# Optimization experiments

Measured on AMD Instinct MI355X. Metric: run time of the kernel, lower is better.

The kernel has to match this reference:

```python
import jax, jax.numpy as jnp
import numpy as np

NUM_HEADS = 16


def setup_inputs() -> dict:
    key = jax.random.key(0)
    k1, k2, k3 = jax.random.split(key, 3)
    B, N, C = 4, 2048, 1024
    x = jax.random.normal(k1, (B, N, C), dtype=jnp.float32)
    w_qkv = jax.random.normal(k2, (C, 3 * C), dtype=jnp.float32) * (C ** -0.5)
    w_proj = jax.random.normal(k3, (C, C), dtype=jnp.float32) * (C ** -0.5)
    b_proj = jnp.zeros((C,), dtype=jnp.float32)
    return {"x": x, "w_qkv": w_qkv, "w_proj": w_proj, "b_proj": b_proj}


def reference(x, w_qkv, w_proj, b_proj):
    B, N, C = x.shape
    H = NUM_HEADS
    hd = C // H
    scale = hd ** -0.5
    # qkv projection (no bias), split into q, k, v per head
    qkv = jnp.einsum('bnc,cd->bnd', x, w_qkv)            # [B, N, 3C]
    qkv = qkv.reshape(B, N, 3, H, hd).transpose(0, 3, 2, 1, 4)  # [B, H, 3, N, hd]
    q, k, v = qkv[:, :, 0], qkv[:, :, 1], qkv[:, :, 2]   # each [B, H, N, hd]
    q = q * scale
    attn = jax.nn.softmax(jnp.einsum('bhnd,bhmd->bhnm', q, k), axis=-1)  # [B, H, N, N]
    out = jnp.einsum('bhnm,bhmd->bhnd', attn, v)         # [B, H, N, hd]
    out = out.transpose(0, 2, 1, 3).reshape(B, N, C)
    return jnp.einsum('bnc,cd->bnd', out, w_proj) + b_proj
```

## Files before the change

### kernel.cpp

```cpp
#include <hip/hip_runtime.h>

typedef short s16x8 __attribute__((ext_vector_type(8)));
typedef float f32x4 __attribute__((ext_vector_type(4)));
typedef float f32x16 __attribute__((ext_vector_type(16)));
typedef unsigned u32x4 __attribute__((ext_vector_type(4)));


__device__ __forceinline__ unsigned short bf16bits(float f) {
  unsigned u = __builtin_bit_cast(unsigned, f);
  unsigned rnd = 0x7FFFu + ((u >> 16) & 1u);
  return (unsigned short)((u + rnd) >> 16);
}

__device__ __forceinline__ unsigned pk_bf16(float lo, float hi) {
  unsigned r;
  asm("v_cvt_pk_bf16_f32 %0, %1, %2" : "=v"(r) : "v"(lo), "v"(hi));
  return r;
}

__device__ __forceinline__ void async16(const void* g, void* l) {
  __builtin_amdgcn_global_load_lds((const __attribute__((address_space(1))) void*)g,
                                   (__attribute__((address_space(3))) void*)l, 16, 0, 0);
}

__device__ __forceinline__ f32x4 mfma16(s16x8 a, s16x8 b, f32x4 c) {
  return __builtin_amdgcn_mfma_f32_16x16x32_bf16(a, b, c, 0, 0, 0);
}

__device__ __forceinline__ f32x16 mfma32(s16x8 a, s16x8 b, f32x16 c) {
  return __builtin_amdgcn_mfma_f32_32x32x16_bf16(a, b, c, 0, 0, 0);
}

__device__ __forceinline__ s16x8 lds_frag(const unsigned short* S, int row, int c8, int U) {
  int unit = row * U + (c8 ^ (row & (U - 1)));
  return *(const s16x8*)(S + unit * 8);
}

__global__ __launch_bounds__(256) void prep(const float4* __restrict__ x4,
                                            unsigned short* __restrict__ Xb,
                                            const float* __restrict__ w_qkv,
                                            unsigned short* __restrict__ Wqt,
                                            const float* __restrict__ w_proj,
                                            unsigned short* __restrict__ Wpt) {
  __shared__ float tile[32][33];
  const int blk = blockIdx.x, t = threadIdx.x;
  if (blk < 2048) {
    const int n4 = 8388608 / 4, stride = 2048 * 256;
    for (int i = blk * 256 + t; i < n4; i += stride) {
      float4 v = x4[i];
      uint2 o;
      o.x = pk_bf16(v.x, v.y);
      o.y = pk_bf16(v.z, v.w);
      *(uint2*)(Xb + (size_t)i * 4) = o;
    }
    return;
  }
  const float* in;
  unsigned short* out;
  int R, C, c0, r0;
  if (blk < 2048 + 3072) {
    int idx = blk - 2048;
    in = w_qkv; out = Wqt; R = 1024; C = 3072;
    c0 = (idx % 96) * 32; r0 = (idx / 96) * 32;
  } else {
    int idx = blk - (2048 + 3072);
    in = w_proj; out = Wpt; R = 1024; C = 1024;
    c0 = (idx & 31) * 32; r0 = (idx >> 5) * 32;
  }
  const int tx = t & 31, ty = t >> 5;
  #pragma unroll
  for (int i = 0; i < 32; i += 8)
    tile[ty + i][tx] = in[(size_t)(r0 + ty + i) * C + c0 + tx];
  __syncthreads();
  #pragma unroll
  for (int i = 0; i < 32; i += 8)
    out[(size_t)(c0 + ty + i) * R + r0 + tx] = bf16bits(tile[tx][ty + i]);
}

__global__ __launch_bounds__(256) void transpose_v(const unsigned short* __restrict__ V,
                                                   unsigned short* __restrict__ Vt) {
  __shared__ unsigned short sm[64 * 68];
  int bh = blockIdx.y, kt0 = blockIdx.x * 64;
  const unsigned short* v = V + (size_t)bh * 2048 * 64 + (size_t)kt0 * 64;
  unsigned short* vt = Vt + (size_t)bh * 64 * 2048;
  int t = threadIdx.x;
  #pragma unroll
  for (int i = 0; i < 4; ++i) {
    int u = i * 256 + t;
    int f = u * 4;
    int k = f >> 6, d0 = f & 63;
    *(uint2*)&sm[k * 68 + d0] = *(const uint2*)&v[f];
  }
  __syncthreads();
  #pragma unroll
  for (int j = 0; j < 16; ++j) {
    int o = j * 256 + t;
    int d = o >> 6, k = o & 63;
    vt[(size_t)d * 2048 + kt0 + k] = sm[k * 68 + d];
  }
}


template <typename EPI>
__global__ __launch_bounds__(512, 2) void gemm8(const unsigned short* __restrict__ A,
                                                const unsigned short* __restrict__ Bt,
                                                int K, EPI epi) {
  __shared__ __align__(16) unsigned short As[3 * 128 * 64];
  __shared__ __align__(16) unsigned short Bs[3 * 256 * 64];
  const int tid = threadIdx.x, wid = tid >> 6, lane = tid & 63;
  const int quad = lane >> 4, l16 = lane & 15;
  const int bm0 = blockIdx.y * 128, bn0 = blockIdx.x * 256;
  const int wm = (wid & 1) * 64, wn = (wid >> 1) * 64;
  const int NT = K >> 6;
  f32x4 acc[4][4] = {};

  const int srow = tid >> 3;
  const int sc8 = (tid & 7) ^ (srow & 7);
  auto stage = [&](int s, int tk, int k) {
    int col = tk * 64 + sc8 * 8;
    if (k < 2)
      async16(A + (size_t)(bm0 + k * 64 + srow) * K + col,
              (char*)As + s * 16384 + k * 8192 + wid * 1024);
    else
      async16(Bt + (size_t)(bn0 + (k - 2) * 64 + srow) * K + col,
              (char*)Bs + s * 32768 + (k - 2) * 8192 + wid * 1024);
  };

  #pragma unroll
  for (int k = 0; k < 6; ++k) stage(0, 0, k);
  #pragma unroll
  for (int k = 0; k < 6; ++k) stage(1, 1, k);
  asm volatile("s_waitcnt vmcnt(6)" ::: "memory");
  __builtin_amdgcn_s_barrier();
  __builtin_amdgcn_sched_barrier(0);

  int sc = 0;
  for (int t = 0; t < NT; ++t) {
    const unsigned short* as = As + sc * 8192;
    const unsigned short* bs = Bs + sc * 16384;
    const int sp = (sc == 0) ? 2 : sc - 1;
    const bool pf = (t + 2 < NT);

    #pragma unroll
    for (int kk = 0; kk < 2; ++kk) {
      s16x8 a[4], b[4];
      #pragma unroll
      for (int i = 0; i < 4; ++i) a[i] = lds_frag(as, wm + i * 16 + l16, kk * 4 + quad, 8);
      #pragma unroll
      for (int j = 0; j < 4; ++j) b[j] = lds_frag(bs, wn + j * 16 + l16, kk * 4 + quad, 8);
      if (pf) { stage(sp, t + 2, kk * 3 + 0); stage(sp, t + 2, kk * 3 + 1); stage(sp, t + 2, kk * 3 + 2); }
      __builtin_amdgcn_sched_barrier(0);
      __builtin_amdgcn_s_barrier();
      __builtin_amdgcn_s_setprio(1);
      #pragma unroll
      for (int i = 0; i < 4; ++i)
        #pragma unroll
        for (int j = 0; j < 4; ++j)
          acc[i][j] = mfma16(a[i], b[j], acc[i][j]);
      __builtin_amdgcn_s_setprio(0);
      __builtin_amdgcn_sched_barrier(0);
      if (kk == 1) {
        if (pf) asm volatile("s_waitcnt vmcnt(6)" ::: "memory");
        else    asm volatile("s_waitcnt vmcnt(0)" ::: "memory");
      }
      __builtin_amdgcn_s_barrier();
    }
    sc = (sc == 2) ? 0 : sc + 1;
  }

  #pragma unroll
  for (int i = 0; i < 4; ++i)
    #pragma unroll
    for (int j = 0; j < 4; ++j)
      epi.store4(bm0 + wm + i * 16 + quad * 4, bn0 + wn + j * 16 + l16, acc[i][j]);
}

struct QKVEpi {
  unsigned short *Q, *K, *V;
  float qscale;
  __device__ __forceinline__ void store4(int m0, int n, f32x4 v) const {
    int s = m0 >> 10, h = (m0 >> 6) & 15, d = m0 & 63;
    int b = n >> 11, ns = n & 2047;
    unsigned short* dst = (s == 0) ? Q : ((s == 1) ? K : V);
    float sc = (s == 0) ? qscale : 1.f;
    uint2 o;
    o.x = pk_bf16(v[0] * sc, v[1] * sc);
    o.y = pk_bf16(v[2] * sc, v[3] * sc);
    *(uint2*)&dst[(((size_t)b * 16 + h) * 2048 + ns) * 64 + d] = o;
  }
};

struct ProjEpi {
  const float* bias;
  float* out;
  __device__ __forceinline__ void store4(int m0, int n, f32x4 v) const {
    float4 b4 = *(const float4*)&bias[m0];
    float4 o = {v[0] + b4.x, v[1] + b4.y, v[2] + b4.z, v[3] + b4.w};
    *(float4*)&out[(size_t)n * 1024 + m0] = o;
  }
};

__global__ __launch_bounds__(256, 4) void flash_attn(const unsigned short* __restrict__ Q,
                                                     const unsigned short* __restrict__ K,
                                                     const unsigned short* __restrict__ Vt,
                                                     unsigned short* __restrict__ O) {
  __shared__ __align__(16) unsigned short Ks[2][8 * 512];
  __shared__ __align__(16) unsigned short Vs[2][8 * 512];
  const int tid = threadIdx.x, wid = tid >> 6, lane = tid & 63;
  const int l31 = lane & 31, half = lane >> 5;
  const int bid = blockIdx.y * gridDim.x + blockIdx.x;
  const int xcd = bid & 7, idx = bid >> 3;
  const int bh = xcd * 8 + (idx & 7);
  const int qt = idx >> 3;
  const unsigned short* Qg = Q + (size_t)bh * 2048 * 64;
  const unsigned short* Kg = K + (size_t)bh * 2048 * 64;
  const unsigned short* Vg = Vt + (size_t)bh * 64 * 2048;
  const int qrow = qt * 128 + wid * 32 + l31;

  s16x8 qB[4];
  #pragma unroll
  for (int s = 0; s < 4; ++s)
    qB[s] = *(const s16x8*)&Qg[(size_t)qrow * 64 + s * 16 + half * 8];

  const bool isK = wid < 2;
  int sA[4];
  #pragma unroll
  for (int t = 0; t < 4; ++t) {
    int c = (wid & 1) * 4 + t;
    if (isK) sA[t] = ((c >> 2) * 32 + l31) * 64 + ((c & 3) * 2 + half) * 8;
    else     sA[t] = ((c & 1) * 32 + l31) * 2048 + (c >> 1) * 16 + half * 8;
  }

  auto stage = [&](int kt, int buf) {
    const int kb = kt * 64;
    #pragma unroll
    for (int t = 0; t < 4; ++t) {
      int c = (wid & 1) * 4 + t;
      if (isK) async16(Kg + (size_t)kb * 64 + sA[t], (char*)&Ks[buf][0] + c * 1024);
      else     async16(Vg + kb + sA[t],              (char*)&Vs[buf][0] + c * 1024);
    }
  };

  f32x16 oacc[2] = {};
  float l_i = 0.f;
  const f32x16 fz = {};

  stage(0, 0);
  for (int kt = 0; kt < 32; ++kt) {
    const int cur = kt & 1;
    __syncthreads();
    if (kt + 1 < 32) stage(kt + 1, cur ^ 1);
    const unsigned short* ks = &Ks[cur][0];
    const unsigned short* vs = &Vs[cur][0];

    f32x16 st[2];
    __builtin_amdgcn_s_setprio(1);
    #pragma unroll
    for (int kf = 0; kf < 2; ++kf) {
      {
        s16x8 a = *(const s16x8*)&ks[((kf * 4 + 0) * 64 + lane) * 8];
        st[kf] = mfma32(a, qB[0], fz);
      }
      #pragma unroll
      for (int s = 1; s < 4; ++s) {
        s16x8 a = *(const s16x8*)&ks[((kf * 4 + s) * 64 + lane) * 8];
        st[kf] = mfma32(a, qB[s], st[kf]);
      }
    }
    __builtin_amdgcn_s_setprio(0);

    #pragma unroll
    for (int kf = 0; kf < 2; ++kf) {
      float a0 = 0.f, a1 = 0.f, a2 = 0.f, a3 = 0.f;
      #pragma unroll
      for (int r = 0; r < 16; r += 4) {
        float p0 = __builtin_amdgcn_exp2f(st[kf][r + 0]);
        float p1 = __builtin_amdgcn_exp2f(st[kf][r + 1]);
        float p2 = __builtin_amdgcn_exp2f(st[kf][r + 2]);
        float p3 = __builtin_amdgcn_exp2f(st[kf][r + 3]);
        st[kf][r + 0] = p0; st[kf][r + 1] = p1; st[kf][r + 2] = p2; st[kf][r + 3] = p3;
        a0 += p0; a1 += p1; a2 += p2; a3 += p3;
      }
      float rs = (a0 + a1) + (a2 + a3);
      rs += __shfl_xor(rs, 32);
      l_i += rs;
      #pragma unroll
      for (int t = 0; t < 2; ++t) {
        int rb = t * 8;
        unsigned pa0 = pk_bf16(st[kf][rb + 0], st[kf][rb + 1]);
        unsigned pa1 = pk_bf16(st[kf][rb + 2], st[kf][rb + 3]);
        unsigned pb0 = pk_bf16(st[kf][rb + 4], st[kf][rb + 5]);
        unsigned pb1 = pk_bf16(st[kf][rb + 6], st[kf][rb + 7]);
        unsigned s0 = half ? pa0 : pb0;
        unsigned s1 = half ? pa1 : pb1;
        unsigned r0 = (unsigned)__shfl_xor((int)s0, 32);
        unsigned r1 = (unsigned)__shfl_xor((int)s1, 32);
        u32x4 bP;
        bP[0] = half ? r0 : pa0;
        bP[1] = half ? r1 : pa1;
        bP[2] = half ? pb0 : r0;
        bP[3] = half ? pb1 : r1;
        __builtin_amdgcn_s_setprio(1);
        #pragma unroll
        for (int f = 0; f < 2; ++f) {
          s16x8 aV = *(const s16x8*)&vs[(((kf * 2 + t) * 2 + f) * 64 + lane) * 8];
          oacc[f] = mfma32(aV, __builtin_bit_cast(s16x8, bP), oacc[f]);
        }
        __builtin_amdgcn_s_setprio(0);
      }
    }
  }

  const int b = bh >> 4, h = bh & 15;
  float inv = 1.f / l_i;
  size_t base = (((size_t)b * 2048 + qrow) * 16 + h) * 64;
  #pragma unroll
  for (int f = 0; f < 2; ++f)
    #pragma unroll
    for (int q = 0; q < 4; ++q) {
      int d0 = f * 32 + q * 8 + half * 4;
      uint2 o;
      o.x = pk_bf16(oacc[f][q * 4 + 0] * inv, oacc[f][q * 4 + 1] * inv);
      o.y = pk_bf16(oacc[f][q * 4 + 2] * inv, oacc[f][q * 4 + 3] * inv);
      *(uint2*)&O[base + d0] = o;
    }
}


extern "C" void kernel_launch(void* const* d_in, const int* in_sizes, int n_in,
                              void* d_out, int out_size, void* d_ws, size_t ws_size,
                              hipStream_t stream) {
  (void)in_sizes; (void)n_in; (void)out_size; (void)ws_size;
  const float* x = (const float*)d_in[0];
  const float* w_qkv = (const float*)d_in[1];
  const float* w_proj = (const float*)d_in[2];
  const float* b_proj = (const float*)d_in[3];
  float* out = (float*)d_out;
  char* ws = (char*)d_ws;
  const size_t MB = 1ull << 20;
  unsigned short* Xb  = (unsigned short*)(ws);
  unsigned short* Wqt = (unsigned short*)(ws + 16 * MB);
  unsigned short* Wpt = (unsigned short*)(ws + 22 * MB);
  unsigned short* Qb  = (unsigned short*)(ws + 24 * MB);
  unsigned short* Kb  = (unsigned short*)(ws + 40 * MB);
  unsigned short* Vb  = (unsigned short*)(ws + 56 * MB);
  unsigned short* Vt  = Xb;
  unsigned short* Ob  = Vb;

  prep<<<2048 + 3072 + 1024, 256, 0, stream>>>((const float4*)x, Xb, w_qkv, Wqt, w_proj, Wpt);

  QKVEpi e1{Qb, Kb, Vb, 0.125f * 1.44269504088896340736f};
  gemm8<QKVEpi><<<dim3(32, 24), 512, 0, stream>>>(Wqt, Xb, 1024, e1);

  transpose_v<<<dim3(32, 64), 256, 0, stream>>>(Vb, Vt);
  flash_attn<<<dim3(16, 64), 256, 0, stream>>>(Qb, Kb, Vt, Ob);

  ProjEpi e2{b_proj, out};
  gemm8<ProjEpi><<<dim3(32, 8), 512, 0, stream>>>(Wpt, Ob, 1024, e2);
}
```

Baseline: 278.7 us.

## Process two 32-row query groups per wave in flash attention to reuse K/V fragments

Each wave now handles 64 query rows (two 32-row groups) instead of 32, so every K and V fragment read from LDS feeds two MFMAs. The query tile per block doubles to 256, the grid halves, and launch bounds drop to 2 blocks per CU to allow the extra registers. This cuts LDS traffic and K/V staging per query row, at the cost of higher register pressure, lower occupancy, and fewer blocks to fill the GPU.

```diff
diff --git a/kernel.cpp b/kernel.cpp
--- a/kernel.cpp
+++ b/kernel.cpp
@@ -200,7 +200,7 @@
   }
 };
 
-__global__ __launch_bounds__(256, 4) void flash_attn(const unsigned short* __restrict__ Q,
+__global__ __launch_bounds__(256, 2) void flash_attn(const unsigned short* __restrict__ Q,
                                                      const unsigned short* __restrict__ K,
                                                      const unsigned short* __restrict__ Vt,
                                                      unsigned short* __restrict__ O) {
@@ -215,12 +215,15 @@
   const unsigned short* Qg = Q + (size_t)bh * 2048 * 64;
   const unsigned short* Kg = K + (size_t)bh * 2048 * 64;
   const unsigned short* Vg = Vt + (size_t)bh * 64 * 2048;
-  const int qrow = qt * 128 + wid * 32 + l31;
-
-  s16x8 qB[4];
-  #pragma unroll
-  for (int s = 0; s < 4; ++s)
-    qB[s] = *(const s16x8*)&Qg[(size_t)qrow * 64 + s * 16 + half * 8];
+  const int qrow0 = qt * 256 + wid * 64 + l31;
+  const int qrow1 = qrow0 + 32;
+
+  s16x8 qB[2][4];
+  #pragma unroll
+  for (int s = 0; s < 4; ++s) {
+    qB[0][s] = *(const s16x8*)&Qg[(size_t)qrow0 * 64 + s * 16 + half * 8];
+    qB[1][s] = *(const s16x8*)&Qg[(size_t)qrow1 * 64 + s * 16 + half * 8];
+  }
 
   const bool isK = wid < 2;
   int sA[4];
@@ -241,8 +244,8 @@
     }
   };
 
-  f32x16 oacc[2] = {};
-  float l_i = 0.f;
+  f32x16 oacc[2][2] = {};
+  float l_i[2] = {0.f, 0.f};
   const f32x16 fz = {};
 
   stage(0, 0);
@@ -253,58 +256,63 @@
     const unsigned short* ks = &Ks[cur][0];
     const unsigned short* vs = &Vs[cur][0];
 
-    f32x16 st[2];
-    __builtin_amdgcn_s_setprio(1);
     #pragma unroll
     for (int kf = 0; kf < 2; ++kf) {
+      f32x16 st[2];
+      __builtin_amdgcn_s_setprio(1);
       {
         s16x8 a = *(const s16x8*)&ks[((kf * 4 + 0) * 64 + lane) * 8];
-        st[kf] = mfma32(a, qB[0], fz);
+        st[0] = mfma32(a, qB[0][0], fz);
+        st[1] = mfma32(a, qB[1][0], fz);
       }
       #pragma unroll
       for (int s = 1; s < 4; ++s) {
         s16x8 a = *(const s16x8*)&ks[((kf * 4 + s) * 64 + lane) * 8];
-        st[kf] = mfma32(a, qB[s], st[kf]);
-      }
-    }
-    __builtin_amdgcn_s_setprio(0);
-
-    #pragma unroll
-    for (int kf = 0; kf < 2; ++kf) {
-      float a0 = 0.f, a1 = 0.f, a2 = 0.f, a3 = 0.f;
-      #pragma unroll
-      for (int r = 0; r < 16; r += 4) {
-        float p0 = __builtin_amdgcn_exp2f(st[kf][r + 0]);
-        float p1 = __builtin_amdgcn_exp2f(st[kf][r + 1]);
-        float p2 = __builtin_amdgcn_exp2f(st[kf][r + 2]);
-        float p3 = __builtin_amdgcn_exp2f(st[kf][r + 3]);
-        st[kf][r + 0] = p0; st[kf][r + 1] = p1; st[kf][r + 2] = p2; st[kf][r + 3] = p3;
-        a0 += p0; a1 += p1; a2 += p2; a3 += p3;
-      }
-      float rs = (a0 + a1) + (a2 + a3);
-      rs += __shfl_xor(rs, 32);
-      l_i += rs;
+        st[0] = mfma32(a, qB[0][s], st[0]);
+        st[1] = mfma32(a, qB[1][s], st[1]);
+      }
+      __builtin_amdgcn_s_setprio(0);
+      #pragma unroll
+      for (int g = 0; g < 2; ++g) {
+        float a0 = 0.f, a1 = 0.f, a2 = 0.f, a3 = 0.f;
+        #pragma unroll
+        for (int r = 0; r < 16; r += 4) {
+          float p0 = __builtin_amdgcn_exp2f(st[g][r + 0]);
+          float p1 = __builtin_amdgcn_exp2f(st[g][r + 1]);
+          float p2 = __builtin_amdgcn_exp2f(st[g][r + 2]);
+          float p3 = __builtin_amdgcn_exp2f(st[g][r + 3]);
+          st[g][r + 0] = p0; st[g][r + 1] = p1; st[g][r + 2] = p2; st[g][r + 3] = p3;
+          a0 += p0; a1 += p1; a2 += p2; a3 += p3;
+        }
+        float rs = (a0 + a1) + (a2 + a3);
+        rs += __shfl_xor(rs, 32);
+        l_i[g] += rs;
+      }
       #pragma unroll
       for (int t = 0; t < 2; ++t) {
         int rb = t * 8;
-        unsigned pa0 = pk_bf16(st[kf][rb + 0], st[kf][rb + 1]);
-        unsigned pa1 = pk_bf16(st[kf][rb + 2], st[kf][rb + 3]);
-        unsigned pb0 = pk_bf16(st[kf][rb + 4], st[kf][rb + 5]);
-        unsigned pb1 = pk_bf16(st[kf][rb + 6], st[kf][rb + 7]);
-        unsigned s0 = half ? pa0 : pb0;
-        unsigned s1 = half ? pa1 : pb1;
-        unsigned r0 = (unsigned)__shfl_xor((int)s0, 32);
-        unsigned r1 = (unsigned)__shfl_xor((int)s1, 32);
-        u32x4 bP;
-        bP[0] = half ? r0 : pa0;
-        bP[1] = half ? r1 : pa1;
-        bP[2] = half ? pb0 : r0;
-        bP[3] = half ? pb1 : r1;
+        u32x4 bP[2];
+        #pragma unroll
+        for (int g = 0; g < 2; ++g) {
+          unsigned pa0 = pk_bf16(st[g][rb + 0], st[g][rb + 1]);
+          unsigned pa1 = pk_bf16(st[g][rb + 2], st[g][rb + 3]);
+          unsigned pb0 = pk_bf16(st[g][rb + 4], st[g][rb + 5]);
+          unsigned pb1 = pk_bf16(st[g][rb + 6], st[g][rb + 7]);
+          unsigned s0 = half ? pa0 : pb0;
+          unsigned s1 = half ? pa1 : pb1;
+          unsigned r0 = (unsigned)__shfl_xor((int)s0, 32);
+          unsigned r1 = (unsigned)__shfl_xor((int)s1, 32);
+          bP[g][0] = half ? r0 : pa0;
+          bP[g][1] = half ? r1 : pa1;
+          bP[g][2] = half ? pb0 : r0;
+          bP[g][3] = half ? pb1 : r1;
+        }
         __builtin_amdgcn_s_setprio(1);
         #pragma unroll
         for (int f = 0; f < 2; ++f) {
           s16x8 aV = *(const s16x8*)&vs[(((kf * 2 + t) * 2 + f) * 64 + lane) * 8];
-          oacc[f] = mfma32(aV, __builtin_bit_cast(s16x8, bP), oacc[f]);
+          oacc[0][f] = mfma32(aV, __builtin_bit_cast(s16x8, bP[0]), oacc[0][f]);
+          oacc[1][f] = mfma32(aV, __builtin_bit_cast(s16x8, bP[1]), oacc[1][f]);
         }
         __builtin_amdgcn_s_setprio(0);
       }
@@ -312,18 +320,22 @@
   }
 
   const int b = bh >> 4, h = bh & 15;
-  float inv = 1.f / l_i;
-  size_t base = (((size_t)b * 2048 + qrow) * 16 + h) * 64;
-  #pragma unroll
-  for (int f = 0; f < 2; ++f)
-    #pragma unroll
-    for (int q = 0; q < 4; ++q) {
-      int d0 = f * 32 + q * 8 + half * 4;
-      uint2 o;
-      o.x = pk_bf16(oacc[f][q * 4 + 0] * inv, oacc[f][q * 4 + 1] * inv);
-      o.y = pk_bf16(oacc[f][q * 4 + 2] * inv, oacc[f][q * 4 + 3] * inv);
-      *(uint2*)&O[base + d0] = o;
-    }
+  #pragma unroll
+  for (int g = 0; g < 2; ++g) {
+    float inv = 1.f / l_i[g];
+    int qrow = g ? qrow1 : qrow0;
+    size_t base = (((size_t)b * 2048 + qrow) * 16 + h) * 64;
+    #pragma unroll
+    for (int f = 0; f < 2; ++f)
+      #pragma unroll
+      for (int q = 0; q < 4; ++q) {
+        int d0 = f * 32 + q * 8 + half * 4;
+        uint2 o;
+        o.x = pk_bf16(oacc[g][f][q * 4 + 0] * inv, oacc[g][f][q * 4 + 1] * inv);
+        o.y = pk_bf16(oacc[g][f][q * 4 + 2] * inv, oacc[g][f][q * 4 + 3] * inv);
+        *(uint2*)&O[base + d0] = o;
+      }
+  }
 }
 
 
@@ -353,7 +365,7 @@
   gemm8<QKVEpi><<<dim3(32, 24), 512, 0, stream>>>(Wqt, Xb, 1024, e1);
 
   transpose_v<<<dim3(32, 64), 256, 0, stream>>>(Vb, Vt);
-  flash_attn<<<dim3(16, 64), 256, 0, stream>>>(Qb, Kb, Vt, Ob);
+  flash_attn<<<dim3(8, 64), 256, 0, stream>>>(Qb, Kb, Vt, Ob);
 
   ProjEpi e2{b_proj, out};
   gemm8<ProjEpi><<<dim3(32, 8), 512, 0, stream>>>(Wpt, Ob, 1024, e2);
```

Measured after the change: 271.2 us. -2.7%, faster.
